# Kernel tuning notes

Hardware: AMD Instinct MI355X
Metric: run time of the kernel (lower is better)

Reference implementation:

```python
import jax, jax.numpy as jnp
import numpy as np

NUM_CLASSES = 22
MARGIN = 0.01  # margin of the hinge on squared point distance


def quat_to_rotmat(q):
    # q: [..., 4] unit quaternion in (w, x, y, z) order -> [..., 3, 3]
    w, x, y, z = q[..., 0], q[..., 1], q[..., 2], q[..., 3]
    return jnp.stack([
        jnp.stack([1 - 2 * (y * y + z * z), 2 * (x * y - z * w), 2 * (x * z + y * w)], -1),
        jnp.stack([2 * (x * y + z * w), 1 - 2 * (x * x + z * z), 2 * (y * z - x * w)], -1),
        jnp.stack([2 * (x * z - y * w), 2 * (y * z + x * w), 1 - 2 * (x * x + y * y)], -1),
    ], -2)


def setup_inputs() -> dict:
    key = jax.random.key(0)
    B, C, P = 128, NUM_CLASSES, 1024
    ks = jax.random.split(key, 5)
    qp = jax.random.normal(ks[0], (B, C, 4), dtype=jnp.float32)
    qp = qp / jnp.linalg.norm(qp, axis=-1, keepdims=True)
    qg = jax.random.normal(ks[1], (B, C, 4), dtype=jnp.float32)
    qg = qg / jnp.linalg.norm(qg, axis=-1, keepdims=True)
    cls = jax.random.randint(ks[2], (B,), 1, C)  # skip background class 0
    poses_weight = jnp.repeat(jax.nn.one_hot(cls, C, dtype=jnp.float32), 4, axis=1)  # [B, 4C]
    points = 0.05 * jax.random.normal(ks[3], (C, P, 3), dtype=jnp.float32)  # object models (~meters)
    symmetry = (jax.random.uniform(ks[4], (C,)) < 0.5).astype(jnp.float32)
    return {
        'poses_pred': qp.reshape(B, 4 * C),
        'poses_target': qg.reshape(B, 4 * C),
        'poses_weight': poses_weight,
        'points': points,
        'symmetry': symmetry,
    }


def reference(poses_pred, poses_target, poses_weight, points, symmetry):
    B = poses_pred.shape[0]
    P = points.shape[1]
    # class selection: first class i with weight[n, 4i] > 0 (as in the CUDA kernel)
    w = poses_weight.reshape(B, NUM_CLASSES, 4)[:, :, 0]
    valid = jnp.any(w > 0, axis=1)
    cls = jnp.argmax(w > 0, axis=1)

    rows = jnp.arange(B)
    q_pred = poses_pred.reshape(B, NUM_CLASSES, 4)[rows, cls]   # [B,4]
    q_gt = poses_target.reshape(B, NUM_CLASSES, 4)[rows, cls]   # [B,4]
    pts = points[cls]                                           # [B,P,3] gather per class
    sym = symmetry[cls] > 0                                     # [B]

    Rp = quat_to_rotmat(q_pred)
    Rg = quat_to_rotmat(q_gt)
    xp = jnp.einsum('bij,bpj->bpi', Rp, pts)  # predicted-pose rotated points [B,P,3]
    xg = jnp.einsum('bij,bpj->bpi', Rg, pts)  # target-pose rotated points   [B,P,3]

    # ADD: matched squared distance
    d_diag = jnp.sum((xp - xg) ** 2, axis=-1)  # [B,P]
    # ADD-S: nearest-neighbor squared distance via ||a||^2 + ||b||^2 - 2 a.b
    d2 = (jnp.sum(xp * xp, -1)[:, :, None] + jnp.sum(xg * xg, -1)[:, None, :]
          - 2.0 * jnp.einsum('bpc,bqc->bpq', xp, xg))  # [B,P,P]
    d_sym = jnp.min(jnp.maximum(d2, 0.0), axis=2)       # [B,P]

    d = jnp.where(sym[:, None], d_sym, d_diag)
    per_point = 0.5 * jnp.maximum(d - MARGIN, 0.0)       # margin-clamped
    per_point = per_point * valid[:, None].astype(per_point.dtype)
    return jnp.sum(per_point) / (B * P)
```

## Files before the change

### kernel.cpp

```cpp
#include <hip/hip_runtime.h>
#include <math.h>

#define NUM_CLASSES 22
#define MARGIN 0.01f
#define PTS 1024
#define BLOCK 256
#define R 8
#define PPT 8
#define PGRP (BLOCK / R)
#define PBLK (PGRP * PPT)
#define SBLK (PTS / PBLK)
#define QT (PTS / R)
#define HSTRIDE (QT + 1)

__device__ __forceinline__ void quat_to_rot(const float* __restrict__ q, float R_[9]) {
    float w = q[0], x = q[1], y = q[2], z = q[3];
    R_[0] = 1.f - 2.f * (y * y + z * z);
    R_[1] = 2.f * (x * y - z * w);
    R_[2] = 2.f * (x * z + y * w);
    R_[3] = 2.f * (x * y + z * w);
    R_[4] = 1.f - 2.f * (x * x + z * z);
    R_[5] = 2.f * (y * z - x * w);
    R_[6] = 2.f * (x * z - y * w);
    R_[7] = 2.f * (y * z + x * w);
    R_[8] = 1.f - 2.f * (x * x + y * y);
}

__global__ __launch_bounds__(BLOCK) void adl_kernel(
    const float* __restrict__ poses_pred,
    const float* __restrict__ poses_target,
    const float* __restrict__ poses_weight,
    const float* __restrict__ points,
    const float* __restrict__ symmetry,
    float* __restrict__ out,
    float inv_scale)
{
    __shared__ float4 s_h[R * HSTRIDE];
    __shared__ float s_part[BLOCK / 64];

    const int b = blockIdx.x / SBLK;
    const int s = blockIdx.x - b * SBLK;
    const int tid = threadIdx.x;
    const int lane = tid & 63;

    const float* wrow = poses_weight + (size_t)b * 4 * NUM_CLASSES;
    float wv = (lane < NUM_CLASSES) ? wrow[4 * lane] : 0.f;
    unsigned long long msk = __ballot(wv > 0.f);
    if (msk == 0ULL) return;
    const int cls = __ffsll((unsigned long long)msk) - 1;

    float Rp[9], Rg[9];
    quat_to_rot(poses_pred + ((size_t)b * NUM_CLASSES + cls) * 4, Rp);
    quat_to_rot(poses_target + ((size_t)b * NUM_CLASSES + cls) * 4, Rg);
    const bool sym = symmetry[cls] > 0.f;
    const float* pts = points + (size_t)cls * PTS * 3;

    float sum = 0.f;

    if (sym) {
        #pragma unroll
        for (int k = 0; k < PTS / BLOCK; ++k) {
            const int Q = tid + k * BLOCK;
            float px = pts[3 * Q + 0];
            float py = pts[3 * Q + 1];
            float pz = pts[3 * Q + 2];
            float gx = Rg[0] * px + Rg[1] * py + Rg[2] * pz;
            float gy = Rg[3] * px + Rg[4] * py + Rg[5] * pz;
            float gz = Rg[6] * px + Rg[7] * py + Rg[8] * pz;
            s_h[(Q >> 7) * HSTRIDE + (Q & (QT - 1))] =
                make_float4(-2.f * gx, -2.f * gy, -2.f * gz,
                            gx * gx + gy * gy + gz * gz);
        }
        __syncthreads();

        const int qq = tid & (R - 1);
        const int pg = tid >> 3;

        float ax[PPT], ay[PPT], az[PPT], na[PPT], m[PPT];
        #pragma unroll
        for (int j = 0; j < PPT; ++j) {
            const int p = s * PBLK + pg + j * PGRP;
            float px = pts[3 * p + 0];
            float py = pts[3 * p + 1];
            float pz = pts[3 * p + 2];
            ax[j] = Rp[0] * px + Rp[1] * py + Rp[2] * pz;
            ay[j] = Rp[3] * px + Rp[4] * py + Rp[5] * pz;
            az[j] = Rp[6] * px + Rp[7] * py + Rp[8] * pz;
            na[j] = ax[j] * ax[j] + ay[j] * ay[j] + az[j] * az[j];
            m[j] = INFINITY;
        }

        const float4* __restrict__ hq = s_h + qq * HSTRIDE;
        float4 h = hq[0];
        #pragma unroll 4
        for (int q = 0; q < QT; ++q) {
            float4 hn = hq[q + 1];
            #pragma unroll
            for (int j = 0; j < PPT; ++j) {
                float t = fmaf(az[j], h.z, h.w);
                t = fmaf(ay[j], h.y, t);
                t = fmaf(ax[j], h.x, t);
                m[j] = fminf(m[j], t);
            }
            h = hn;
        }

        #pragma unroll
        for (int j = 0; j < PPT; ++j) {
            #pragma unroll
            for (int d = 1; d < R; d <<= 1)
                m[j] = fminf(m[j], __shfl_xor(m[j], d, 64));
        }
        if (qq == 0) {
            #pragma unroll
            for (int j = 0; j < PPT; ++j)
                sum += 0.5f * fmaxf(na[j] + m[j] - MARGIN, 0.f);
        }
    } else {
        const int p = s * PBLK + tid;
        float px = pts[3 * p + 0];
        float py = pts[3 * p + 1];
        float pz = pts[3 * p + 2];
        float axv = Rp[0] * px + Rp[1] * py + Rp[2] * pz;
        float ayv = Rp[3] * px + Rp[4] * py + Rp[5] * pz;
        float azv = Rp[6] * px + Rp[7] * py + Rp[8] * pz;
        float gx = Rg[0] * px + Rg[1] * py + Rg[2] * pz;
        float gy = Rg[3] * px + Rg[4] * py + Rg[5] * pz;
        float gz = Rg[6] * px + Rg[7] * py + Rg[8] * pz;
        float dx = axv - gx, dy = ayv - gy, dz = azv - gz;
        float d = dx * dx + dy * dy + dz * dz;
        sum = 0.5f * fmaxf(d - MARGIN, 0.f);
    }

    #pragma unroll
    for (int off = 32; off > 0; off >>= 1)
        sum += __shfl_down(sum, off, 64);
    const int wave = tid >> 6;
    if (lane == 0) s_part[wave] = sum;
    __syncthreads();
    if (tid == 0) {
        float total = 0.f;
        #pragma unroll
        for (int w = 0; w < BLOCK / 64; ++w) total += s_part[w];
        atomicAdd(out, total * inv_scale);
    }
}

extern "C" void kernel_launch(void* const* d_in, const int* in_sizes, int n_in,
                              void* d_out, int out_size, void* d_ws, size_t ws_size,
                              hipStream_t stream) {
    const float* poses_pred   = (const float*)d_in[0];
    const float* poses_target = (const float*)d_in[1];
    const float* poses_weight = (const float*)d_in[2];
    const float* points       = (const float*)d_in[3];
    const float* symmetry     = (const float*)d_in[4];
    float* out = (float*)d_out;

    const int B = in_sizes[0] / (4 * NUM_CLASSES);
    const float inv_scale = 1.0f / ((float)B * (float)PTS);

    adl_kernel<<<B * SBLK, BLOCK, 0, stream>>>(
        poses_pred, poses_target, poses_weight, points, symmetry, out, inv_scale);
}
```

Before: 74.03 us.

## Add planning kernel to compact sym/non-sym work and widen query split

Adds a single-block planning kernel that picks each batch's class and builds compacted lists of symmetric and non-symmetric samples in the workspace. The main kernel then launches exactly SBLK blocks per symmetric sample and one block per non-symmetric sample, which now covers all 1024 points in a loop. This replaces the old scheme where non-symmetric samples spread over many lightly loaded blocks. R goes from 8 to 16, which halves the query slice per thread and raises SBLK, with a 16-lane min reduction. The cost is an extra kernel launch plus a workspace round trip, and surplus blocks in the grid exit early.

```diff
diff --git a/kernel.cpp b/kernel.cpp
--- a/kernel.cpp
+++ b/kernel.cpp
@@ -5,13 +5,14 @@
 #define MARGIN 0.01f
 #define PTS 1024
 #define BLOCK 256
-#define R 8
+#define R 16
 #define PPT 8
 #define PGRP (BLOCK / R)
 #define PBLK (PGRP * PPT)
 #define SBLK (PTS / PBLK)
 #define QT (PTS / R)
 #define HSTRIDE (QT + 1)
+
 
 __device__ __forceinline__ void quat_to_rot(const float* __restrict__ q, float R_[9]) {
     float w = q[0], x = q[1], y = q[2], z = q[3];
@@ -26,33 +27,71 @@
     R_[8] = 1.f - 2.f * (x * x + y * y);
 }
 
+__global__ __launch_bounds__(1024) void plan_kernel(
+    const float* __restrict__ poses_weight,
+    const float* __restrict__ symmetry,
+    unsigned* __restrict__ ws,
+    int B)
+{
+    __shared__ unsigned cnt[2];
+    const int b = threadIdx.x;
+    if (b < 2) cnt[b] = 0;
+    __syncthreads();
+    if (b < B) {
+        const float* wrow = poses_weight + (size_t)b * 4 * NUM_CLASSES;
+        int cls = -1;
+        #pragma unroll
+        for (int c = NUM_CLASSES - 1; c >= 0; --c)
+            if (wrow[4 * c] > 0.f) cls = c;
+        if (cls >= 0) {
+            const bool sym = symmetry[cls] > 0.f;
+            const unsigned slot = atomicAdd(&cnt[sym ? 0 : 1], 1u);
+            const unsigned entry = ((unsigned)b << 5) | (unsigned)cls;
+            if (sym) ws[2 + slot] = entry;
+            else     ws[2 + (unsigned)B + slot] = entry;
+        }
+    }
+    __syncthreads();
+    if (b == 0) { ws[0] = cnt[0]; ws[1] = cnt[1]; }
+}
+
 __global__ __launch_bounds__(BLOCK) void adl_kernel(
     const float* __restrict__ poses_pred,
     const float* __restrict__ poses_target,
-    const float* __restrict__ poses_weight,
     const float* __restrict__ points,
-    const float* __restrict__ symmetry,
     float* __restrict__ out,
+    const unsigned* __restrict__ ws,
+    int B,
     float inv_scale)
 {
     __shared__ float4 s_h[R * HSTRIDE];
     __shared__ float s_part[BLOCK / 64];
 
-    const int b = blockIdx.x / SBLK;
-    const int s = blockIdx.x - b * SBLK;
+    const unsigned g = blockIdx.x;
+    const unsigned nsymblk = ws[0] * SBLK;
+
+    unsigned entry;
+    int s = 0;
+    bool sym;
+    if (g < nsymblk) {
+        entry = ws[2 + (g >> 3)];
+        s = (int)(g & 7u);
+        sym = true;
+    } else {
+        const unsigned j = g - nsymblk;
+        if (j >= ws[1]) return;
+        entry = ws[2 + (unsigned)B + j];
+        sym = false;
+    }
+    const int b = (int)(entry >> 5);
+    const int cls = (int)(entry & 31u);
+
     const int tid = threadIdx.x;
     const int lane = tid & 63;
-
-    const float* wrow = poses_weight + (size_t)b * 4 * NUM_CLASSES;
-    float wv = (lane < NUM_CLASSES) ? wrow[4 * lane] : 0.f;
-    unsigned long long msk = __ballot(wv > 0.f);
-    if (msk == 0ULL) return;
-    const int cls = __ffsll((unsigned long long)msk) - 1;
 
     float Rp[9], Rg[9];
     quat_to_rot(poses_pred + ((size_t)b * NUM_CLASSES + cls) * 4, Rp);
     quat_to_rot(poses_target + ((size_t)b * NUM_CLASSES + cls) * 4, Rg);
-    const bool sym = symmetry[cls] > 0.f;
     const float* pts = points + (size_t)cls * PTS * 3;
 
     float sum = 0.f;
@@ -67,14 +106,14 @@
             float gx = Rg[0] * px + Rg[1] * py + Rg[2] * pz;
             float gy = Rg[3] * px + Rg[4] * py + Rg[5] * pz;
             float gz = Rg[6] * px + Rg[7] * py + Rg[8] * pz;
-            s_h[(Q >> 7) * HSTRIDE + (Q & (QT - 1))] =
+            s_h[(Q >> 6) * HSTRIDE + (Q & (QT - 1))] =
                 make_float4(-2.f * gx, -2.f * gy, -2.f * gz,
                             gx * gx + gy * gy + gz * gz);
         }
         __syncthreads();
 
         const int qq = tid & (R - 1);
-        const int pg = tid >> 3;
+        const int pg = tid >> 4;
 
         float ax[PPT], ay[PPT], az[PPT], na[PPT], m[PPT];
         #pragma unroll
@@ -117,19 +156,22 @@
                 sum += 0.5f * fmaxf(na[j] + m[j] - MARGIN, 0.f);
         }
     } else {
-        const int p = s * PBLK + tid;
-        float px = pts[3 * p + 0];
-        float py = pts[3 * p + 1];
-        float pz = pts[3 * p + 2];
-        float axv = Rp[0] * px + Rp[1] * py + Rp[2] * pz;
-        float ayv = Rp[3] * px + Rp[4] * py + Rp[5] * pz;
-        float azv = Rp[6] * px + Rp[7] * py + Rp[8] * pz;
-        float gx = Rg[0] * px + Rg[1] * py + Rg[2] * pz;
-        float gy = Rg[3] * px + Rg[4] * py + Rg[5] * pz;
-        float gz = Rg[6] * px + Rg[7] * py + Rg[8] * pz;
-        float dx = axv - gx, dy = ayv - gy, dz = azv - gz;
-        float d = dx * dx + dy * dy + dz * dz;
-        sum = 0.5f * fmaxf(d - MARGIN, 0.f);
+        #pragma unroll
+        for (int k = 0; k < PTS / BLOCK; ++k) {
+            const int p = tid + k * BLOCK;
+            float px = pts[3 * p + 0];
+            float py = pts[3 * p + 1];
+            float pz = pts[3 * p + 2];
+            float axv = Rp[0] * px + Rp[1] * py + Rp[2] * pz;
+            float ayv = Rp[3] * px + Rp[4] * py + Rp[5] * pz;
+            float azv = Rp[6] * px + Rp[7] * py + Rp[8] * pz;
+            float gx = Rg[0] * px + Rg[1] * py + Rg[2] * pz;
+            float gy = Rg[3] * px + Rg[4] * py + Rg[5] * pz;
+            float gz = Rg[6] * px + Rg[7] * py + Rg[8] * pz;
+            float dx = axv - gx, dy = ayv - gy, dz = azv - gz;
+            float d = dx * dx + dy * dy + dz * dz;
+            sum += 0.5f * fmaxf(d - MARGIN, 0.f);
+        }
     }
 
     #pragma unroll
@@ -159,6 +201,7 @@
     const int B = in_sizes[0] / (4 * NUM_CLASSES);
     const float inv_scale = 1.0f / ((float)B * (float)PTS);
 
-    adl_kernel<<<B * SBLK, BLOCK, 0, stream>>>(
-        poses_pred, poses_target, poses_weight, points, symmetry, out, inv_scale);
-}
+    plan_kernel<<<1, B, 0, stream>>>(poses_weight, symmetry, (unsigned*)d_ws, B);
+    adl_kernel<<<(unsigned)(B * (SBLK + 1)), BLOCK, 0, stream>>>(
+        poses_pred, poses_target, points, out, (const unsigned*)d_ws, B, inv_scale);
+}
```

New measurement: 75.84 us. 1.02x slower.
